# Optimization experiments

Hardware: AMD Instinct MI355X
Metric: run time of the kernel (lower is better)

## Reference

```python
import jax, jax.numpy as jnp
import numpy as np

V, D, NS, H, L, B, T = 96, 256, 24, 512, 2, 64, 128
TAU = 1.0


def setup_inputs() -> dict:
    key = jax.random.key(0)
    ks = jax.random.split(key, 20)

    def nrm(k, shape, s=0.02):
        return (jax.random.normal(k, shape, jnp.float32) * s).astype(jnp.float32)

    return {
        "x": jax.random.randint(ks[0], (B, T), 0, V),
        "emb": nrm(ks[1], (V, D)),
        "pos_emb": nrm(ks[2], (1024, D)),
        # per-layer params stacked on leading L axis; Linear weights stored (in, out)
        "route_w1": nrm(ks[3], (L, 2 * D, D)),
        "route_b1": jnp.zeros((L, D), jnp.float32),
        "route_w2": nrm(ks[4], (L, D, NS)),
        "route_b2": jnp.zeros((L, NS), jnp.float32),
        # GRUCell: weight_ih/hh are [3D, D] (r,z,n gate order, torch layout)
        "gru_wih": nrm(ks[5], (L, 3 * D, D), 0.5 / np.sqrt(D)),
        "gru_whh": nrm(ks[6], (L, 3 * D, D), 0.5 / np.sqrt(D)),
        "gru_bih": jnp.zeros((L, 3 * D), jnp.float32),
        "gru_bhh": jnp.zeros((L, 3 * D), jnp.float32),
        "proj_w": nrm(ks[7], (L, D, D)),
        "proj_b": jnp.zeros((L, D), jnp.float32),
        "ln1_g": jnp.ones((L, D), jnp.float32),
        "ln1_b": jnp.zeros((L, D), jnp.float32),
        "ffn_w1": nrm(ks[8], (L, D, H)),
        "ffn_b1": jnp.zeros((L, H), jnp.float32),
        "ffn_w2": nrm(ks[9], (L, H, D)),
        "ffn_b2": jnp.zeros((L, D), jnp.float32),
        "ln2_g": jnp.ones((L, D), jnp.float32),
        "ln2_b": jnp.zeros((L, D), jnp.float32),
        "lnout_g": jnp.ones((D,), jnp.float32),
        "lnout_b": jnp.zeros((D,), jnp.float32),
        "head_w": nrm(ks[10], (D, V)),
        "head_b": jnp.zeros((V,), jnp.float32),
    }


def _layernorm(v, g, b, eps=1e-5):
    m = v.mean(-1, keepdims=True)
    c = v - m
    var = (c * c).mean(-1, keepdims=True)
    return c * jax.lax.rsqrt(var + eps) * g + b


def reference(x, emb, pos_emb, route_w1, route_b1, route_w2, route_b2,
              gru_wih, gru_whh, gru_bih, gru_bhh, proj_w, proj_b,
              ln1_g, ln1_b, ffn_w1, ffn_b1, ffn_w2, ffn_b2, ln2_g, ln2_b,
              lnout_g, lnout_b, head_w, head_b):

    def block(xv, S, i):
        # xv: [B, D], S: [B, NS, D]
        slot_mean = S.mean(axis=1)                                   # [B, D]
        ctx = jnp.concatenate([xv, slot_mean], axis=-1)              # [B, 2D]
        hmid = jax.nn.gelu(ctx @ route_w1[i] + route_b1[i], approximate=False)
        alpha = jax.nn.softmax((hmid @ route_w2[i] + route_b2[i]) / TAU, axis=-1)  # [B, NS]
        U = alpha[..., None] * xv[:, None, :]                        # [B, NS, D]
        # GRUCell on flattened (B*NS) "batch"
        gi = jnp.einsum('bsd,ed->bse', U, gru_wih[i]) + gru_bih[i]   # [B, NS, 3D]
        gh = jnp.einsum('bsd,ed->bse', S, gru_whh[i]) + gru_bhh[i]
        ir, iz, in_ = jnp.split(gi, 3, axis=-1)
        hr, hz, hn = jnp.split(gh, 3, axis=-1)
        r = jax.nn.sigmoid(ir + hr)
        z = jax.nn.sigmoid(iz + hz)
        n = jnp.tanh(in_ + r * hn)
        S_new = (1.0 - z) * n + z * S                                # [B, NS, D]
        slot_ctx = jnp.einsum('bs,bsd->bd', alpha, S_new)            # [B, D]
        x_mid = xv + slot_ctx @ proj_w[i] + proj_b[i]
        h1 = _layernorm(x_mid, ln1_g[i], ln1_b[i])
        ff = jax.nn.gelu(h1 @ ffn_w1[i] + ffn_b1[i], approximate=False) @ ffn_w2[i] + ffn_b2[i]
        x_out = _layernorm(x_mid + ff, ln2_g[i], ln2_b[i])
        return x_out, S_new

    def step(S_stack, inp):
        tok, p = inp                                                 # tok: [B], p: [D]
        xv = emb[tok] + p
        new_S = []
        for i in range(L):
            xv, Si = block(xv, S_stack[i], i)
            new_S.append(Si)
        logits_t = _layernorm(xv, lnout_g, lnout_b) @ head_w + head_b  # [B, V]
        return jnp.stack(new_S), logits_t

    S0 = jnp.zeros((L, x.shape[0], NS, D), jnp.float32)
    _, logits = jax.lax.scan(step, S0, (x.T, pos_emb[:x.shape[1]]))  # logits: [T, B, V]
    return jnp.transpose(logits, (1, 0, 2))                          # [B, T, V]
```

## Files before the change

### kernel.cpp

```cpp
#include <hip/hip_runtime.h>
#include <hip/hip_fp16.h>

typedef unsigned short u16;
typedef _Float16 f16x8 __attribute__((ext_vector_type(8)));
typedef float f32x4 __attribute__((ext_vector_type(4)));

#define VV   96
#define DD   256
#define NSL  24
#define HH   512
#define LL   2
#define BB   64
#define TT   128

#define EXB    3489792u
#define SBYT   45056u
#define OF_R2P 0u
#define OF_PJP 1024u
#define OF_F2P 9216u
#define OF_SM  17408u
#define OF_S16 19456u
#define OF_FLAGS (EXB + 64u*SBYT)

#define AG_ST(p,v) __hip_atomic_store((p),(v),__ATOMIC_RELAXED,__HIP_MEMORY_SCOPE_AGENT)
#define AG_LD(p)   __hip_atomic_load((p),__ATOMIC_RELAXED,__HIP_MEMORY_SCOPE_AGENT)

__device__ __forceinline__ u16 f2h(float f){ return __half_as_ushort(__float2half(f)); }
__device__ __forceinline__ float h2f(u16 u){ return __half2float(__ushort_as_half(u)); }
__device__ __forceinline__ float gelu_f(float x){ return 0.5f*x*(1.f+erff(x*0.70710678118654752f)); }
__device__ __forceinline__ float sigm_f(float x){ return 1.f/(1.f+__expf(-x)); }
__device__ __forceinline__ float tanh_f(float x){
  x = fminf(15.f, fmaxf(-15.f, x));
  float e2 = __expf(2.f*x);
  return (e2-1.f)/(e2+1.f);
}

__device__ __forceinline__ float dotg8(const u16* __restrict__ row, const float* __restrict__ v,
                                       int g, int iters){
  float acc = 0.f;
  #pragma unroll
  for(int it=0; it<iters; ++it){
    int k = (it*8 + g)*8;
    uint4 w = *(const uint4*)(row + k);
    float4 a  = *(const float4*)(v + k);
    float4 bq = *(const float4*)(v + k + 4);
    float2 f0 = __half22float2(*(const __half2*)&w.x);
    float2 f1 = __half22float2(*(const __half2*)&w.y);
    float2 f2_ = __half22float2(*(const __half2*)&w.z);
    float2 f3 = __half22float2(*(const __half2*)&w.w);
    acc += f0.x*a.x + f0.y*a.y + f1.x*a.z + f1.y*a.w;
    acc += f2_.x*bq.x + f2_.y*bq.y + f3.x*bq.z + f3.y*bq.w;
  }
  return acc;
}
__device__ __forceinline__ float dotg16(const u16* __restrict__ row, const float* __restrict__ v,
                                        int tl, int iters){
  float acc = 0.f;
  #pragma unroll
  for(int it=0; it<iters; ++it){
    int k = (it*16 + tl)*8;
    uint4 w = *(const uint4*)(row + k);
    float4 a  = *(const float4*)(v + k);
    float4 bq = *(const float4*)(v + k + 4);
    float2 f0 = __half22float2(*(const __half2*)&w.x);
    float2 f1 = __half22float2(*(const __half2*)&w.y);
    float2 f2_ = __half22float2(*(const __half2*)&w.z);
    float2 f3 = __half22float2(*(const __half2*)&w.w);
    acc += f0.x*a.x + f0.y*a.y + f1.x*a.z + f1.y*a.w;
    acc += f2_.x*bq.x + f2_.y*bq.y + f3.x*bq.z + f3.y*bq.w;
  }
  return acc;
}
__device__ __forceinline__ float red8(float a){
  a += __shfl_down(a,4,64); a += __shfl_down(a,2,64); a += __shfl_down(a,1,64);
  return a;
}
__device__ __forceinline__ float red16(float a){
  a += __shfl_down(a,8,64); a += __shfl_down(a,4,64);
  a += __shfl_down(a,2,64); a += __shfl_down(a,1,64);
  return a;
}

__device__ __forceinline__ void syncq(unsigned* flags, int b, int c, unsigned ep, int tid){
  __syncthreads();
  if(tid==0){
    AG_ST(&flags[b*4+c], ep);
    #pragma unroll
    for(int i=0;i<3;++i){
      int p = i + (i>=c ? 1 : 0);
      while(AG_LD(&flags[b*4+p]) < ep){ __builtin_amdgcn_s_sleep(1); }
    }
  }
  __syncthreads();
}

__global__ void k_cvt(const float* __restrict__ s, u16* __restrict__ d, int n){
  int i = blockIdx.x*256 + threadIdx.x;
  if(i<n) d[i] = f2h(s[i]);
}
__global__ void k_cvtT(const float* __restrict__ s, u16* __restrict__ d, int K, int N){
  int i = blockIdx.x*256 + threadIdx.x;
  if(i < K*N){ int k = i/N, n = i - k*N; d[n*K + k] = f2h(s[i]); }
}
__global__ void k_zeroflags(unsigned* f){ f[threadIdx.x] = 0u; }

__device__ __forceinline__ void layernorm256(float* __restrict__ dst, const float* __restrict__ src,
    const float* __restrict__ g, const float* __restrict__ bta, float* __restrict__ red, int tid){
  float v = (tid < DD) ? src[tid] : 0.f;
  float s1 = v, s2 = v*v;
  #pragma unroll
  for(int o=32;o>0;o>>=1){ s1 += __shfl_down(s1,o,64); s2 += __shfl_down(s2,o,64); }
  if((tid&63)==0){ red[tid>>6] = s1; red[16+(tid>>6)] = s2; }
  __syncthreads();
  if(tid==0){
    float a=0.f,cs=0.f;
    #pragma unroll
    for(int i=0;i<4;++i){ a+=red[i]; cs+=red[16+i]; }
    float m = a*(1.f/DD);
    float var = cs*(1.f/DD) - m*m;
    red[32]=m; red[33]=rsqrtf(var+1e-5f);
  }
  __syncthreads();
  if(tid<DD) dst[tid] = (src[tid]-red[32])*red[33]*g[tid] + bta[tid];
  __syncthreads();
}

__global__ __launch_bounds__(1024, 4) void ssr_main(
    const int* __restrict__ x, const float* __restrict__ emb, const float* __restrict__ pos,
    const u16* __restrict__ r1T, const float* __restrict__ b_r1,
    const u16* __restrict__ r2T, const float* __restrict__ b_r2,
    const u16* __restrict__ wihW, const u16* __restrict__ whhW,
    const float* __restrict__ bih, const float* __restrict__ bhh,
    const u16* __restrict__ pjT, const float* __restrict__ b_pj,
    const float* __restrict__ g1, const float* __restrict__ be1,
    const u16* __restrict__ f1T, const float* __restrict__ b_f1,
    const u16* __restrict__ f2T, const float* __restrict__ b_f2,
    const float* __restrict__ g2, const float* __restrict__ be2,
    const float* __restrict__ go, const float* __restrict__ bo,
    const u16* __restrict__ hdT, const float* __restrict__ b_hd,
    void* __restrict__ wsraw,
    float* __restrict__ out)
{
  extern __shared__ float sm[];
  float* S_l   = sm;
  u16*  sbf    = (u16*)(sm + 3072);
  float* gh_l  = sm + 7296;
  float* gx_l  = sm + 12096;
  float* ctx   = sm + 12288;
  float* xv    = sm + 12800;
  float* xm    = sm + 13056;
  float* h1    = sm + 13312;
  float* hmid_l= sm + 13568;
  float* ff_l  = sm + 13632;
  float* sctx  = sm + 13760;
  float* alpha = sm + 13824;
  float* red   = sm + 13856;
  float* pc    = sm + 13920;

  const int wgid = blockIdx.x;
  const int b = wgid & 63;
  const int c = wgid >> 6;
  const int tid = threadIdx.x;
  const int g = tid & 7,  gid = tid >> 3;
  const int tl = tid & 15, tm = tid >> 4;

  char* exb = (char*)wsraw + EXB + (size_t)b*SBYT;
  float*    ex_r2p = (float*)(exb + OF_R2P);
  float*    ex_pjp = (float*)(exb + OF_PJP);
  float*    ex_f2p = (float*)(exb + OF_F2P);
  float*    ex_sm  = (float*)(exb + OF_SM);
  unsigned* ex_s16 = (unsigned*)(exb + OF_S16);
  unsigned* flags  = (unsigned*)((char*)wsraw + OF_FLAGS);
  unsigned ep = 0;

  for(int i=tid;i<3072;i+=1024) S_l[i]=0.f;
  for(int i=tid;i<4224;i+=1024) ((float*)sbf)[i]=0.f;
  __syncthreads();

  for(int t=0;t<TT;++t){
    const int tok = x[b*TT + t];
    if(tid<DD) xv[tid] = emb[tok*DD+tid] + pos[t*DD+tid];
    __syncthreads();

    for(int li=0; li<LL; ++li){
      if(t>0){
        for(int i=tid;i<3072;i+=1024){
          int s_=i>>7, dw=i&127;
          unsigned d32 = AG_LD(&ex_s16[li*3072+i]);
          *(unsigned*)(sbf + s_*264 + dw*2) = d32;
        }
        if(tid<DD) ctx[DD+tid] = AG_LD(&ex_sm[li*DD+tid]);
      } else {
        if(tid<DD) ctx[DD+tid] = 0.f;
      }
      if(tid<DD) ctx[tid] = xv[tid];
      __syncthreads();

      {
        const u16* row = r1T + (size_t)(li*DD + c*64 + tm)*(2*DD);
        float a = red16(dotg16(row, ctx, tl, 4));
        if(!tl) hmid_l[tm] = gelu_f(a + b_r1[li*DD + c*64 + tm]);
      }
      __syncthreads();
      if(gid < NSL){
        const u16* row = r2T + (size_t)(li*NSL + gid)*DD + c*64;
        float a = red8(dotg8(row, hmid_l, g, 1));
        if(!g) AG_ST(&ex_r2p[li*96 + c*24 + gid], a);
      }
      {
        const u16* W = wihW + (size_t)li*3*DD*DD;
        for(int le=gid; le<192; le+=128){
          int e = (le>>6)*DD + c*64 + (le&63);
          float a = red8(dotg8(W + (size_t)e*DD, xv, g, 4));
          if(!g) gx_l[le] = a;
        }
      }
      {
        const int lane = tid & 63, w = tid >> 6;
        if(w < 12){
          const int lr = lane & 15, lk = lane >> 4;
          const int q = w >> 2, j = w & 3;
          const u16* WB = whhW + (size_t)li*3*DD*DD;
          const u16* a0p = sbf + lr*264 + lk*8;
          const u16* a1p = sbf + (16+lr)*264 + lk*8;
          const u16* bp = WB + (size_t)(q*DD + c*64 + j*16 + lr)*DD + lk*8;
          f32x4 acc0 = {0.f,0.f,0.f,0.f}, acc1 = {0.f,0.f,0.f,0.f};
          #pragma unroll
          for(int ks=0; ks<8; ++ks){
            f16x8 bfr = *(const f16x8*)(bp + ks*32);
            f16x8 a0  = *(const f16x8*)(a0p + ks*32);
            f16x8 a1  = *(const f16x8*)(a1p + ks*32);
            acc0 = __builtin_amdgcn_mfma_f32_16x16x32_f16(a0, bfr, acc0, 0,0,0);
            acc1 = __builtin_amdgcn_mfma_f32_16x16x32_f16(a1, bfr, acc1, 0,0,0);
          }
          int le = q*64 + j*16 + lr;
          #pragma unroll
          for(int r=0;r<4;++r){
            int s0 = lk*4 + r;
            gh_l[s0*200 + le] = acc0[r];
            int s1 = 16 + lk*4 + r;
            if(s1 < NSL) gh_l[s1*200 + le] = acc1[r];
          }
        }
      }
      syncq(flags, b, c, ++ep, tid);
      if(tid < NSL){
        float lg = b_r2[li*NSL+tid];
        #pragma unroll
        for(int cc=0;cc<4;++cc) lg += AG_LD(&ex_r2p[li*96 + cc*24 + tid]);
        alpha[tid] = lg;
      }
      __syncthreads();
      if(tid==0){
        float m=-1e30f;
        for(int s_=0;s_<NSL;++s_) m = fmaxf(m, alpha[s_]);
        float sum=0.f;
        for(int s_=0;s_<NSL;++s_){ float e=__expf(alpha[s_]-m); alpha[s_]=e; sum+=e; }
        float inv = 1.f/sum;
        for(int s_=0;s_<NSL;++s_) alpha[s_]*=inv;
      }
      __syncthreads();
      {
        int dd = tid & 63, sg = tid >> 6;
        int dglob = li*3*DD + c*64 + dd;
        float gir = gx_l[dd],      bir = bih[dglob],        bhr = bhh[dglob];
        float giz = gx_l[64+dd],   biz = bih[dglob+DD],     bhz = bhh[dglob+DD];
        float gin = gx_l[128+dd],  bin = bih[dglob+2*DD],   bhn = bhh[dglob+2*DD];
        float pctx = 0.f;
        float* Sll = S_l + li*NSL*64;
        #pragma unroll
        for(int h=0;h<2;++h){
          int s_ = sg + h*16;
          if(s_ < NSL){
            float al = alpha[s_];
            float hr = gh_l[s_*200 + dd]       + bhr;
            float hz = gh_l[s_*200 + 64 + dd]  + bhz;
            float hn = gh_l[s_*200 + 128 + dd] + bhn;
            float rr = sigm_f(al*gir + bir + hr);
            float zz = sigm_f(al*giz + biz + hz);
            float nn = tanh_f(al*gin + bin + rr*hn);
            float sv = Sll[s_*64+dd];
            float ns = (1.f-zz)*nn + zz*sv;
            Sll[s_*64+dd] = ns;
            pctx += al*ns;
          }
        }
        pc[tid] = pctx;
      }
      __syncthreads();
      if(tid<64){
        float s_=0.f;
        #pragma unroll
        for(int k=0;k<16;++k) s_ += pc[k*64+tid];
        sctx[tid] = s_;
        float m_=0.f;
        const float* Sll = S_l + li*NSL*64;
        #pragma unroll
        for(int s2=0;s2<NSL;++s2) m_ += Sll[s2*64+tid];
        AG_ST(&ex_sm[li*DD + c*64 + tid], m_*(1.f/NSL));
      }
      __syncthreads();
      for(int i=tid;i<768;i+=1024){
        int s_ = i>>5, dp = (i&31)*2;
        const float* Sll = S_l + li*NSL*64;
        unsigned lo = (unsigned)f2h(Sll[s_*64+dp]);
        unsigned hi = (unsigned)f2h(Sll[s_*64+dp+1]);
        AG_ST(&ex_s16[li*3072 + s_*128 + c*32 + (i&31)], lo | (hi<<16));
      }
      {
        #pragma unroll
        for(int p=0;p<2;++p){
          int dout = p*128 + gid;
          const u16* row = pjT + (size_t)(li*DD + dout)*DD + c*64;
          float a = red8(dotg8(row, sctx, g, 1));
          if(!g) AG_ST(&ex_pjp[li*1024 + c*256 + dout], a);
        }
      }
      syncq(flags, b, c, ++ep, tid);
      if(tid<DD){
        float s_ = b_pj[li*DD+tid];
        #pragma unroll
        for(int cc=0;cc<4;++cc) s_ += AG_LD(&ex_pjp[li*1024 + cc*256 + tid]);
        xm[tid] = xv[tid] + s_;
      }
      __syncthreads();
      layernorm256(h1, xm, g1+li*DD, be1+li*DD, red, tid);
      if(gid < 128){
        const u16* row = f1T + (size_t)(li*HH + c*128 + gid)*DD;
        float a = red8(dotg8(row, h1, g, 4));
        if(!g) ff_l[gid] = gelu_f(a + b_f1[li*HH + c*128 + gid]);
      }
      __syncthreads();
      {
        #pragma unroll
        for(int p=0;p<4;++p){
          int dout = p*64 + tm;
          const u16* row = f2T + (size_t)(li*DD + dout)*HH + c*128;
          float a = red16(dotg16(row, ff_l, tl, 1));
          if(!tl) AG_ST(&ex_f2p[li*1024 + c*256 + dout], a);
        }
      }
      syncq(flags, b, c, ++ep, tid);
      if(tid<DD){
        float s_ = b_f2[li*DD+tid];
        #pragma unroll
        for(int cc=0;cc<4;++cc) s_ += AG_LD(&ex_f2p[li*1024 + cc*256 + tid]);
        xm[tid] = xm[tid] + s_;
      }
      __syncthreads();
      layernorm256(xv, xm, g2+li*DD, be2+li*DD, red, tid);
    }

    layernorm256(h1, xv, go, bo, red, tid);
    if(gid < NSL){
      int n = c*24 + gid;
      float acc = red8(dotg8(hdT + (size_t)n*DD, h1, g, 4));
      if(!g) out[((size_t)b*TT + t)*VV + n] = acc + b_hd[n];
    }
    __syncthreads();
  }
}

extern "C" void kernel_launch(void* const* d_in, const int* in_sizes, int n_in,
                              void* d_out, int out_size, void* d_ws, size_t ws_size,
                              hipStream_t stream){
  const int*   x    = (const int*)  d_in[0];
  const float* emb  = (const float*)d_in[1];
  const float* pos  = (const float*)d_in[2];
  const float* r1   = (const float*)d_in[3];
  const float* br1  = (const float*)d_in[4];
  const float* r2   = (const float*)d_in[5];
  const float* br2  = (const float*)d_in[6];
  const float* wih  = (const float*)d_in[7];
  const float* whh  = (const float*)d_in[8];
  const float* bih  = (const float*)d_in[9];
  const float* bhh  = (const float*)d_in[10];
  const float* pj   = (const float*)d_in[11];
  const float* bpj  = (const float*)d_in[12];
  const float* g1   = (const float*)d_in[13];
  const float* be1  = (const float*)d_in[14];
  const float* f1   = (const float*)d_in[15];
  const float* bf1  = (const float*)d_in[16];
  const float* f2   = (const float*)d_in[17];
  const float* bf2  = (const float*)d_in[18];
  const float* g2   = (const float*)d_in[19];
  const float* be2  = (const float*)d_in[20];
  const float* go   = (const float*)d_in[21];
  const float* bo   = (const float*)d_in[22];
  const float* hd   = (const float*)d_in[23];
  const float* bhd  = (const float*)d_in[24];
  float* out = (float*)d_out;
  u16* ws = (u16*)d_ws;

  u16* r1T  = ws + 0;
  u16* r2T  = ws + 262144;
  u16* wihW = ws + 274432;
  u16* whhW = ws + 667648;
  u16* pjT  = ws + 1060864;
  u16* f1T  = ws + 1191936;
  u16* f2T  = ws + 1454080;
  u16* hdT  = ws + 1716224;

  k_cvt<<<(2*768*256+255)/256,256,0,stream>>>(wih, wihW, 2*768*256);
  k_cvt<<<(2*768*256+255)/256,256,0,stream>>>(whh, whhW, 2*768*256);
  for(int li=0; li<2; ++li){
    k_cvtT<<<(512*256+255)/256,256,0,stream>>>(r1 + li*512*256, r1T + li*256*512, 512, 256);
    k_cvtT<<<(256*24+255)/256, 256,0,stream>>>(r2 + li*256*24,  r2T + li*24*256,  256, 24);
    k_cvtT<<<(256*256+255)/256,256,0,stream>>>(pj + li*256*256, pjT + li*256*256, 256, 256);
    k_cvtT<<<(256*512+255)/256,256,0,stream>>>(f1 + li*256*512, f1T + li*512*256, 256, 512);
    k_cvtT<<<(512*256+255)/256,256,0,stream>>>(f2 + li*512*256, f2T + li*256*512, 512, 256);
  }
  k_cvtT<<<(256*96+255)/256,256,0,stream>>>(hd, hdT, 256, 96);
  k_zeroflags<<<1,256,0,stream>>>((unsigned*)((char*)d_ws + OF_FLAGS));

  const int smem = 14944*4;
  hipFuncSetAttribute(reinterpret_cast<const void*>(ssr_main),
                      hipFuncAttributeMaxDynamicSharedMemorySize, smem);
  ssr_main<<<4*BB, 1024, smem, stream>>>(x, emb, pos, r1T, br1, r2T, br2, wihW, whhW, bih, bhh,
                                         pjT, bpj, g1, be1, f1T, bf1, f2T, bf2, g2, be2, go, bo,
                                         hdT, bhd, d_ws, out);
}
```

Measured before the change: 5.537 ms.

## Cut block barriers with single-wave layernorm/softmax and prefetch both layers' slot state

Replaces the block-wide layernorm (three __syncthreads plus a single-thread reduction) with single-wavefront layernorms fused with the cross-block partial-sum gather. The serial softmax becomes a wave-shuffle softmax. The GRU update now runs in one wave that also computes the slot mean and writes the packed fp16 slot export directly, which removes two barrier phases. Each step prefetches both layers' slot states into double-buffered LDS, and syncq polls peer flags from three threads in parallel. The trade-off is that a single 64-thread wave now serially handles all 24 slots in the GRU update, and shared memory use grows.

```diff
diff --git a/kernel.cpp b/kernel.cpp
--- a/kernel.cpp
+++ b/kernel.cpp
@@ -26,7 +26,6 @@
 #define AG_LD(p)   __hip_atomic_load((p),__ATOMIC_RELAXED,__HIP_MEMORY_SCOPE_AGENT)
 
 __device__ __forceinline__ u16 f2h(float f){ return __half_as_ushort(__float2half(f)); }
-__device__ __forceinline__ float h2f(u16 u){ return __half2float(__ushort_as_half(u)); }
 __device__ __forceinline__ float gelu_f(float x){ return 0.5f*x*(1.f+erff(x*0.70710678118654752f)); }
 __device__ __forceinline__ float sigm_f(float x){ return 1.f/(1.f+__expf(-x)); }
 __device__ __forceinline__ float tanh_f(float x){
@@ -83,13 +82,10 @@
 
 __device__ __forceinline__ void syncq(unsigned* flags, int b, int c, unsigned ep, int tid){
   __syncthreads();
-  if(tid==0){
-    AG_ST(&flags[b*4+c], ep);
-    #pragma unroll
-    for(int i=0;i<3;++i){
-      int p = i + (i>=c ? 1 : 0);
-      while(AG_LD(&flags[b*4+p]) < ep){ __builtin_amdgcn_s_sleep(1); }
-    }
+  if(tid==0) AG_ST(&flags[b*4+c], ep);
+  if(tid<3){
+    int p = tid + (tid>=c ? 1 : 0);
+    while(AG_LD(&flags[b*4+p]) < ep){ __builtin_amdgcn_s_sleep(1); }
   }
   __syncthreads();
 }
@@ -103,27 +99,6 @@
   if(i < K*N){ int k = i/N, n = i - k*N; d[n*K + k] = f2h(s[i]); }
 }
 __global__ void k_zeroflags(unsigned* f){ f[threadIdx.x] = 0u; }
-
-__device__ __forceinline__ void layernorm256(float* __restrict__ dst, const float* __restrict__ src,
-    const float* __restrict__ g, const float* __restrict__ bta, float* __restrict__ red, int tid){
-  float v = (tid < DD) ? src[tid] : 0.f;
-  float s1 = v, s2 = v*v;
-  #pragma unroll
-  for(int o=32;o>0;o>>=1){ s1 += __shfl_down(s1,o,64); s2 += __shfl_down(s2,o,64); }
-  if((tid&63)==0){ red[tid>>6] = s1; red[16+(tid>>6)] = s2; }
-  __syncthreads();
-  if(tid==0){
-    float a=0.f,cs=0.f;
-    #pragma unroll
-    for(int i=0;i<4;++i){ a+=red[i]; cs+=red[16+i]; }
-    float m = a*(1.f/DD);
-    float var = cs*(1.f/DD) - m*m;
-    red[32]=m; red[33]=rsqrtf(var+1e-5f);
-  }
-  __syncthreads();
-  if(tid<DD) dst[tid] = (src[tid]-red[32])*red[33]*g[tid] + bta[tid];
-  __syncthreads();
-}
 
 __global__ __launch_bounds__(1024, 4) void ssr_main(
     const int* __restrict__ x, const float* __restrict__ emb, const float* __restrict__ pos,
@@ -143,19 +118,18 @@
 {
   extern __shared__ float sm[];
   float* S_l   = sm;
-  u16*  sbf    = (u16*)(sm + 3072);
-  float* gh_l  = sm + 7296;
-  float* gx_l  = sm + 12096;
-  float* ctx   = sm + 12288;
-  float* xv    = sm + 12800;
-  float* xm    = sm + 13056;
-  float* h1    = sm + 13312;
-  float* hmid_l= sm + 13568;
-  float* ff_l  = sm + 13632;
-  float* sctx  = sm + 13760;
-  float* alpha = sm + 13824;
-  float* red   = sm + 13856;
-  float* pc    = sm + 13920;
+  u16*  sbf0   = (u16*)(sm + 3072);
+  u16*  sbf1   = (u16*)(sm + 7296);
+  float* gh_l  = sm + 11520;
+  float* gx_l  = sm + 16320;
+  float* xv    = sm + 16512;
+  float* smean = sm + 16768;
+  float* xm    = sm + 17280;
+  float* h1    = sm + 17536;
+  float* hmid_l= sm + 17792;
+  float* ff_l  = sm + 17856;
+  float* sctx  = sm + 17984;
+  float* alpha = sm + 18048;
 
   const int wgid = blockIdx.x;
   const int b = wgid & 63;
@@ -173,32 +147,34 @@
   unsigned* flags  = (unsigned*)((char*)wsraw + OF_FLAGS);
   unsigned ep = 0;
 
-  for(int i=tid;i<3072;i+=1024) S_l[i]=0.f;
-  for(int i=tid;i<4224;i+=1024) ((float*)sbf)[i]=0.f;
+  for(int i=tid;i<18080;i+=1024) sm[i]=0.f;
   __syncthreads();
 
   for(int t=0;t<TT;++t){
-    const int tok = x[b*TT + t];
-    if(tid<DD) xv[tid] = emb[tok*DD+tid] + pos[t*DD+tid];
+    {
+      const int tok = x[b*TT + t];
+      if(tid<DD) xv[tid] = emb[tok*DD+tid] + pos[t*DD+tid];
+      if(t>0){
+        for(int i=tid;i<6144;i+=1024){
+          int lii = i>>11; lii = i/3072;
+          int j = i - lii*3072;
+          int s_ = j>>7, dw = j&127;
+          unsigned d32 = AG_LD(&ex_s16[i]);
+          u16* dst = (lii ? sbf1 : sbf0) + s_*264 + dw*2;
+          *(unsigned*)dst = d32;
+        }
+        if(tid<512) smean[tid] = AG_LD(&ex_sm[tid]);
+      }
+    }
     __syncthreads();
 
     for(int li=0; li<LL; ++li){
-      if(t>0){
-        for(int i=tid;i<3072;i+=1024){
-          int s_=i>>7, dw=i&127;
-          unsigned d32 = AG_LD(&ex_s16[li*3072+i]);
-          *(unsigned*)(sbf + s_*264 + dw*2) = d32;
-        }
-        if(tid<DD) ctx[DD+tid] = AG_LD(&ex_sm[li*DD+tid]);
-      } else {
-        if(tid<DD) ctx[DD+tid] = 0.f;
-      }
-      if(tid<DD) ctx[tid] = xv[tid];
-      __syncthreads();
-
+      u16* sbf = li ? sbf1 : sbf0;
+      const float* smeanL = smean + li*DD;
       {
         const u16* row = r1T + (size_t)(li*DD + c*64 + tm)*(2*DD);
-        float a = red16(dotg16(row, ctx, tl, 4));
+        float a = dotg16(row, xv, tl, 2) + dotg16(row + 256, smeanL, tl, 2);
+        a = red16(a);
         if(!tl) hmid_l[tm] = gelu_f(a + b_r1[li*DD + c*64 + tm]);
       }
       __syncthreads();
@@ -244,69 +220,50 @@
         }
       }
       syncq(flags, b, c, ++ep, tid);
-      if(tid < NSL){
-        float lg = b_r2[li*NSL+tid];
-        #pragma unroll
-        for(int cc=0;cc<4;++cc) lg += AG_LD(&ex_r2p[li*96 + cc*24 + tid]);
-        alpha[tid] = lg;
-      }
-      __syncthreads();
-      if(tid==0){
-        float m=-1e30f;
-        for(int s_=0;s_<NSL;++s_) m = fmaxf(m, alpha[s_]);
-        float sum=0.f;
-        for(int s_=0;s_<NSL;++s_){ float e=__expf(alpha[s_]-m); alpha[s_]=e; sum+=e; }
-        float inv = 1.f/sum;
-        for(int s_=0;s_<NSL;++s_) alpha[s_]*=inv;
-      }
-      __syncthreads();
-      {
-        int dd = tid & 63, sg = tid >> 6;
-        int dglob = li*3*DD + c*64 + dd;
-        float gir = gx_l[dd],      bir = bih[dglob],        bhr = bhh[dglob];
-        float giz = gx_l[64+dd],   biz = bih[dglob+DD],     bhz = bhh[dglob+DD];
-        float gin = gx_l[128+dd],  bin = bih[dglob+2*DD],   bhn = bhh[dglob+2*DD];
-        float pctx = 0.f;
+      if(tid < 32){
+        float lg = -1e30f;
+        if(tid < NSL){
+          lg = b_r2[li*NSL+tid];
+          #pragma unroll
+          for(int cc=0;cc<4;++cc) lg += AG_LD(&ex_r2p[li*96 + cc*24 + tid]);
+        }
+        float m = lg;
+        #pragma unroll
+        for(int o=16;o>0;o>>=1) m = fmaxf(m, __shfl_xor(m,o,32));
+        float e = (tid<NSL) ? __expf(lg-m) : 0.f;
+        float s = e;
+        #pragma unroll
+        for(int o=16;o>0;o>>=1) s += __shfl_xor(s,o,32);
+        if(tid<NSL) alpha[tid] = e/s;
+      }
+      __syncthreads();
+      if(tid < 64){
+        const int dd = tid;
+        const int dg = li*3*DD + c*64 + dd;
+        float gir=gx_l[dd],     bir=bih[dg],       bhr=bhh[dg];
+        float giz=gx_l[64+dd],  biz=bih[dg+DD],    bhz=bhh[dg+DD];
+        float gin=gx_l[128+dd], bin=bih[dg+2*DD],  bhn=bhh[dg+2*DD];
         float* Sll = S_l + li*NSL*64;
-        #pragma unroll
-        for(int h=0;h<2;++h){
-          int s_ = sg + h*16;
-          if(s_ < NSL){
-            float al = alpha[s_];
-            float hr = gh_l[s_*200 + dd]       + bhr;
-            float hz = gh_l[s_*200 + 64 + dd]  + bhz;
-            float hn = gh_l[s_*200 + 128 + dd] + bhn;
-            float rr = sigm_f(al*gir + bir + hr);
-            float zz = sigm_f(al*giz + biz + hz);
-            float nn = tanh_f(al*gin + bin + rr*hn);
-            float sv = Sll[s_*64+dd];
-            float ns = (1.f-zz)*nn + zz*sv;
-            Sll[s_*64+dd] = ns;
-            pctx += al*ns;
-          }
-        }
-        pc[tid] = pctx;
-      }
-      __syncthreads();
-      if(tid<64){
-        float s_=0.f;
-        #pragma unroll
-        for(int k=0;k<16;++k) s_ += pc[k*64+tid];
-        sctx[tid] = s_;
-        float m_=0.f;
-        const float* Sll = S_l + li*NSL*64;
-        #pragma unroll
-        for(int s2=0;s2<NSL;++s2) m_ += Sll[s2*64+tid];
-        AG_ST(&ex_sm[li*DD + c*64 + tid], m_*(1.f/NSL));
-      }
-      __syncthreads();
-      for(int i=tid;i<768;i+=1024){
-        int s_ = i>>5, dp = (i&31)*2;
-        const float* Sll = S_l + li*NSL*64;
-        unsigned lo = (unsigned)f2h(Sll[s_*64+dp]);
-        unsigned hi = (unsigned)f2h(Sll[s_*64+dp+1]);
-        AG_ST(&ex_s16[li*3072 + s_*128 + c*32 + (i&31)], lo | (hi<<16));
-      }
+        float pctx=0.f, msum=0.f;
+        for(int s_=0;s_<NSL;++s_){
+          float al = alpha[s_];
+          float hr = gh_l[s_*200+dd]      + bhr;
+          float hz = gh_l[s_*200+64+dd]   + bhz;
+          float hn = gh_l[s_*200+128+dd]  + bhn;
+          float rr = sigm_f(al*gir + bir + hr);
+          float zz = sigm_f(al*giz + biz + hz);
+          float nn = tanh_f(al*gin + bin + rr*hn);
+          float ns = (1.f-zz)*nn + zz*Sll[s_*64+dd];
+          Sll[s_*64+dd] = ns;
+          pctx += al*ns; msum += ns;
+          unsigned h = (unsigned)f2h(ns);
+          unsigned o = (unsigned)__shfl_xor((int)h, 1, 64);
+          if(!(dd&1)) AG_ST(&ex_s16[li*3072 + s_*128 + c*32 + (dd>>1)], h | (o<<16));
+        }
+        sctx[dd] = pctx;
+        AG_ST(&ex_sm[li*DD + c*64 + dd], msum*(1.f/NSL));
+      }
+      __syncthreads();
       {
         #pragma unroll
         for(int p=0;p<2;++p){
@@ -317,14 +274,26 @@
         }
       }
       syncq(flags, b, c, ++ep, tid);
-      if(tid<DD){
-        float s_ = b_pj[li*DD+tid];
-        #pragma unroll
-        for(int cc=0;cc<4;++cc) s_ += AG_LD(&ex_pjp[li*1024 + cc*256 + tid]);
-        xm[tid] = xv[tid] + s_;
-      }
-      __syncthreads();
-      layernorm256(h1, xm, g1+li*DD, be1+li*DD, red, tid);
+      if(tid < 64){
+        float vx[4]; float s1=0.f, s2=0.f;
+        #pragma unroll
+        for(int j=0;j<4;++j){
+          int d = j*64 + tid;
+          float p = AG_LD(&ex_pjp[li*1024 + d])     + AG_LD(&ex_pjp[li*1024 + 256 + d])
+                  + AG_LD(&ex_pjp[li*1024 + 512 + d]) + AG_LD(&ex_pjp[li*1024 + 768 + d]);
+          float v = xv[d] + b_pj[li*DD+d] + p;
+          xm[d] = v; vx[j] = v; s1 += v; s2 += v*v;
+        }
+        #pragma unroll
+        for(int o=32;o>0;o>>=1){ s1 += __shfl_xor(s1,o,64); s2 += __shfl_xor(s2,o,64); }
+        float m = s1*(1.f/DD), rs = rsqrtf(s2*(1.f/DD) - m*m + 1e-5f);
+        #pragma unroll
+        for(int j=0;j<4;++j){
+          int d = j*64 + tid;
+          h1[d] = (vx[j]-m)*rs*g1[li*DD+d] + be1[li*DD+d];
+        }
+      }
+      __syncthreads();
       if(gid < 128){
         const u16* row = f1T + (size_t)(li*HH + c*128 + gid)*DD;
         float a = red8(dotg8(row, h1, g, 4));
@@ -341,17 +310,46 @@
         }
       }
       syncq(flags, b, c, ++ep, tid);
-      if(tid<DD){
-        float s_ = b_f2[li*DD+tid];
-        #pragma unroll
-        for(int cc=0;cc<4;++cc) s_ += AG_LD(&ex_f2p[li*1024 + cc*256 + tid]);
-        xm[tid] = xm[tid] + s_;
-      }
-      __syncthreads();
-      layernorm256(xv, xm, g2+li*DD, be2+li*DD, red, tid);
+      if(tid < 64){
+        float vx[4]; float s1=0.f, s2=0.f;
+        #pragma unroll
+        for(int j=0;j<4;++j){
+          int d = j*64 + tid;
+          float p = AG_LD(&ex_f2p[li*1024 + d])       + AG_LD(&ex_f2p[li*1024 + 256 + d])
+                  + AG_LD(&ex_f2p[li*1024 + 512 + d]) + AG_LD(&ex_f2p[li*1024 + 768 + d]);
+          float v = xm[d] + b_f2[li*DD+d] + p;
+          vx[j] = v; s1 += v; s2 += v*v;
+        }
+        #pragma unroll
+        for(int o=32;o>0;o>>=1){ s1 += __shfl_xor(s1,o,64); s2 += __shfl_xor(s2,o,64); }
+        float m = s1*(1.f/DD), rs = rsqrtf(s2*(1.f/DD) - m*m + 1e-5f);
+        #pragma unroll
+        for(int j=0;j<4;++j){
+          int d = j*64 + tid;
+          xv[d] = (vx[j]-m)*rs*g2[li*DD+d] + be2[li*DD+d];
+        }
+      }
+      __syncthreads();
     }
 
-    layernorm256(h1, xv, go, bo, red, tid);
+    if(tid < 64){
+      float vx[4]; float s1=0.f, s2=0.f;
+      #pragma unroll
+      for(int j=0;j<4;++j){
+        int d = j*64 + tid;
+        float v = xv[d];
+        vx[j] = v; s1 += v; s2 += v*v;
+      }
+      #pragma unroll
+      for(int o=32;o>0;o>>=1){ s1 += __shfl_xor(s1,o,64); s2 += __shfl_xor(s2,o,64); }
+      float m = s1*(1.f/DD), rs = rsqrtf(s2*(1.f/DD) - m*m + 1e-5f);
+      #pragma unroll
+      for(int j=0;j<4;++j){
+        int d = j*64 + tid;
+        h1[d] = (vx[j]-m)*rs*go[d] + bo[d];
+      }
+    }
+    __syncthreads();
     if(gid < NSL){
       int n = c*24 + gid;
       float acc = red8(dotg8(hdT + (size_t)n*DD, h1, g, 4));
@@ -413,7 +411,7 @@
   k_cvtT<<<(256*96+255)/256,256,0,stream>>>(hd, hdT, 256, 96);
   k_zeroflags<<<1,256,0,stream>>>((unsigned*)((char*)d_ws + OF_FLAGS));
 
-  const int smem = 14944*4;
+  const int smem = 18080*4;
   hipFuncSetAttribute(reinterpret_cast<const void*>(ssr_main),
                       hipFuncAttributeMaxDynamicSharedMemorySize, smem);
   ssr_main<<<4*BB, 1024, smem, stream>>>(x, emb, pos, r1T, br1, r2T, br2, wihW, whhW, bih, bhh,
```

Result: slower. 7.881 ms (+42.3%).
